# Optimization experiments

Hardware: AMD Instinct MI355X
Metric: run time of the kernel (lower is better)

The kernel has to match this reference:

```python
import jax, jax.numpy as jnp
import numpy as np

N_HEADS = 12


def setup_inputs() -> dict:
    key = jax.random.key(0)
    ks = jax.random.split(key, 3)
    B, N, C = 32, 1024, 768
    x = jax.random.normal(ks[0], (B, N, C), dtype=jnp.float32)
    w_qkv = jax.random.normal(ks[1], (C, 3 * C), dtype=jnp.float32) * (1.0 / np.sqrt(C))
    b_qkv = jnp.zeros((3 * C,), dtype=jnp.float32)
    w_out = jax.random.normal(ks[2], (C, C), dtype=jnp.float32) * (1.0 / np.sqrt(C))
    b_out = jnp.zeros((C,), dtype=jnp.float32)
    return {"x": x, "w_qkv": w_qkv, "b_qkv": b_qkv, "w_out": w_out, "b_out": b_out}


def reference(x, w_qkv, b_qkv, w_out, b_out):
    B, N, C = x.shape
    H = N_HEADS
    D = C // H  # head_dim
    qkv = (x @ w_qkv + b_qkv).reshape(B, N, 3, H, D)
    qkv = jnp.transpose(qkv, (2, 0, 3, 1, 4))
    q, k, v = qkv[0], qkv[1], qkv[2]
    # channel attention: k^T @ v -> (B,H,D,D), scaled by sqrt(head_dim)
    attn = jnp.einsum("bhnd,bhne->bhde", k, v) / np.sqrt(D).astype(np.float32)
    attn = jax.nn.softmax(attn, axis=-1)
    # attn @ q^T -> (B,H,D,N); swapaxes -> (B,H,N,D)
    out = jnp.einsum("bhde,bhne->bhnd", attn, q)
    # ProjOut: merge heads (B,N,C) + Dense(C)
    out = jnp.transpose(out, (0, 2, 1, 3)).reshape(B, N, C)
    return out @ w_out + b_out
```

## Files before the change

kernel.cpp:

```cpp
#include <hip/hip_runtime.h>
#include <hip/hip_bf16.h>
#include <stdint.h>
#include <stddef.h>

#define B_ 32
#define N_ 1024
#define C_ 768
#define H_ 12
#define D_ 64
#define M_ (B_*N_)
#define TC_ (3*C_)

typedef __bf16 bf16_t;
typedef __attribute__((ext_vector_type(8))) __bf16 bf16x8;
typedef __attribute__((ext_vector_type(4))) __bf16 bf16x4;
typedef __attribute__((ext_vector_type(4))) float  f32x4;

#define MFMA16(a,b,c) __builtin_amdgcn_mfma_f32_16x16x32_bf16(a,b,c,0,0,0)

__device__ __forceinline__ void lds_load16(const void* g, void* l) {
  __builtin_amdgcn_global_load_lds(
      (const __attribute__((address_space(1))) void*)g,
      (__attribute__((address_space(3))) void*)l, 16, 0, 0);
}

__global__ void cvt_bf16(const float* __restrict__ in, bf16_t* __restrict__ out, int n) {
  int i = (blockIdx.x * 256 + threadIdx.x) * 8;
  if (i >= n) return;
  const float4 a = *(const float4*)(in + i);
  const float4 b = *(const float4*)(in + i + 4);
  bf16x8 r;
  r[0]=(bf16_t)a.x; r[1]=(bf16_t)a.y; r[2]=(bf16_t)a.z; r[3]=(bf16_t)a.w;
  r[4]=(bf16_t)b.x; r[5]=(bf16_t)b.y; r[6]=(bf16_t)b.z; r[7]=(bf16_t)b.w;
  *(bf16x8*)(out + i) = r;
}

__global__ void transpose_cvt(const float* __restrict__ in, bf16_t* __restrict__ out,
                              int R, int Cc) {
  __shared__ float t[32][33];
  const int c0 = blockIdx.x * 32, r0 = blockIdx.y * 32;
  const int tx = threadIdx.x & 31, ty = threadIdx.x >> 5;
  #pragma unroll
  for (int k = 0; k < 4; ++k)
    t[ty + k*8][tx] = in[(size_t)(r0 + ty + k*8)*Cc + c0 + tx];
  __syncthreads();
  #pragma unroll
  for (int k = 0; k < 4; ++k)
    out[(size_t)(c0 + ty + k*8)*R + r0 + tx] = (bf16_t)t[tx][ty + k*8];
}

template<int MODE>
__global__ __launch_bounds__(512, 2)
void gemm_bt(const bf16_t* __restrict__ A, const bf16_t* __restrict__ BT,
             const float* __restrict__ bias, float* __restrict__ Cout,
             bf16_t* __restrict__ qh,
             bf16_t* __restrict__ kthi, bf16_t* __restrict__ vthi,
             int nbx)
{
  __shared__ __align__(16) char smem[131072];

  const int nwg = gridDim.x;
  const int cpx = nwg >> 3;
  const int bid = blockIdx.x;
  const int swz = (bid & 7) * cpx + (bid >> 3);
  const int bx  = swz % nbx;
  const int by  = swz / nbx;

  const int tid  = threadIdx.x;
  const int wave = tid >> 6;
  const int lane = tid & 63;
  const int rowBase = by * 256;
  const int colBase = bx * 256;
  const int wr = wave >> 2;
  const int wc = wave & 3;
  const int fr = lane & 15;
  const int b   = rowBase >> 10;
  const int nn0 = rowBase & (N_ - 1);

  const int srow = tid >> 2;
  const int scol = (((tid & 3) ^ ((tid >> 2) & 3)) << 3);
  const bf16_t *Ap0, *Ap1, *Bp0, *Bp1;
  if (MODE == 3) {
    Ap0 = A + (size_t)b * (H_*N_*D_) + (size_t)(nn0 + srow) * D_ + scol;
    Ap1 = Ap0 + (size_t)128 * D_;
    const size_t bts = (size_t)b * C_ * C_;
    Bp0 = BT + bts + (size_t)(colBase + srow) * 768 + scol;
    Bp1 = Bp0 + (size_t)128 * 768;
  } else {
    Ap0 = A + (size_t)(rowBase + srow) * 768 + scol;
    Ap1 = Ap0 + (size_t)128 * 768;
    Bp0 = BT + (size_t)(colBase + srow) * 768 + scol;
    Bp1 = Bp0 + (size_t)128 * 768;
  }

  const int chxA = (((lane >> 4) ^ (fr & 3)) << 4);
  const int aoff = (wr*128 + fr)*64 + chxA;
  const int boff = 16384 + (wc*64 + fr)*64 + chxA;

#define RDA(BI,MM) (*(const bf16x8*)(smem + (BI)*32768 + aoff + (MM)*1024))
#define RDB(BI,NN) (*(const bf16x8*)(smem + (BI)*32768 + boff + (NN)*1024))

#define A_OFF(K0) ((MODE == 3) ? ((size_t)((K0) >> 6) << 16) + ((K0) & 32) : (size_t)(K0))

#define STAGE_A(BI, T) do {                                                   \
    const int k0_ = (T) * 32;                                                 \
    const size_t ao_ = A_OFF(k0_);                                            \
    lds_load16(Ap0 + ao_, smem + (BI)*32768 + tid*16);                        \
    lds_load16(Ap1 + ao_, smem + (BI)*32768 + 8192 + tid*16);                 \
  } while (0)

#define STAGE_B(BI, T) do {                                                   \
    const int k0_ = (T) * 32;                                                 \
    lds_load16(Bp0 + k0_, smem + (BI)*32768 + 16384 + tid*16);                \
    lds_load16(Bp1 + k0_, smem + (BI)*32768 + 24576 + tid*16);                \
  } while (0)

  f32x4 acc[8][4];
  #pragma unroll
  for (int m = 0; m < 8; ++m)
    #pragma unroll
    for (int n = 0; n < 4; ++n) acc[m][n] = f32x4{0.f,0.f,0.f,0.f};

#define MFMA_HALF(MB)                                                         \
    acc[MB+0][0]=MFMA16(a0_,b0_,acc[MB+0][0]); acc[MB+0][1]=MFMA16(a0_,b1_,acc[MB+0][1]); \
    acc[MB+0][2]=MFMA16(a0_,b2_,acc[MB+0][2]); acc[MB+0][3]=MFMA16(a0_,b3_,acc[MB+0][3]); \
    acc[MB+1][0]=MFMA16(a1_,b0_,acc[MB+1][0]); acc[MB+1][1]=MFMA16(a1_,b1_,acc[MB+1][1]); \
    acc[MB+1][2]=MFMA16(a1_,b2_,acc[MB+1][2]); acc[MB+1][3]=MFMA16(a1_,b3_,acc[MB+1][3]); \
    acc[MB+2][0]=MFMA16(a2_,b0_,acc[MB+2][0]); acc[MB+2][1]=MFMA16(a2_,b1_,acc[MB+2][1]); \
    acc[MB+2][2]=MFMA16(a2_,b2_,acc[MB+2][2]); acc[MB+2][3]=MFMA16(a2_,b3_,acc[MB+2][3]); \
    acc[MB+3][0]=MFMA16(a3_,b0_,acc[MB+3][0]); acc[MB+3][1]=MFMA16(a3_,b1_,acc[MB+3][1]); \
    acc[MB+3][2]=MFMA16(a3_,b2_,acc[MB+3][2]); acc[MB+3][3]=MFMA16(a3_,b3_,acc[MB+3][3]);

#define TILE(BI, T, DOST, VM) do {                                            \
    asm volatile("s_waitcnt vmcnt(" #VM ")" ::: "memory");                    \
    __builtin_amdgcn_sched_barrier(0);                                        \
    __builtin_amdgcn_s_barrier();                                             \
    __builtin_amdgcn_sched_barrier(0);                                        \
    if (DOST) { STAGE_A(((BI)+3)&3, (T)+3); }                                 \
    __builtin_amdgcn_sched_barrier(0);                                        \
    bf16x8 b0_=RDB(BI,0), b1_=RDB(BI,1), b2_=RDB(BI,2), b3_=RDB(BI,3);        \
    bf16x8 a0_=RDA(BI,0), a1_=RDA(BI,1), a2_=RDA(BI,2), a3_=RDA(BI,3);        \
    __builtin_amdgcn_s_setprio(1);                                            \
    MFMA_HALF(0)                                                              \
    __builtin_amdgcn_s_setprio(0);                                            \
    if (DOST) { STAGE_B(((BI)+3)&3, (T)+3); }                                 \
    __builtin_amdgcn_sched_barrier(0);                                        \
    a0_=RDA(BI,4); a1_=RDA(BI,5); a2_=RDA(BI,6); a3_=RDA(BI,7);               \
    __builtin_amdgcn_s_setprio(1);                                            \
    MFMA_HALF(4)                                                              \
    __builtin_amdgcn_s_setprio(0);                                            \
    asm volatile("s_waitcnt lgkmcnt(0)" ::: "memory");                        \
    __builtin_amdgcn_sched_barrier(0);                                        \
  } while (0)

  STAGE_A(0,0); STAGE_B(0,0);
  STAGE_A(1,1); STAGE_B(1,1);
  STAGE_A(2,2); STAGE_B(2,2);

  #pragma unroll 1
  for (int t = 0; t < 20; t += 4) {
    TILE(0, t,   1, 8);
    TILE(1, t+1, 1, 8);
    TILE(2, t+2, 1, 8);
    TILE(3, t+3, 1, 8);
  }
  TILE(0, 20, 1, 8);
  TILE(1, 21, 0, 8);
  TILE(2, 22, 0, 4);
  TILE(3, 23, 0, 0);

#undef TILE
#undef MFMA_HALF
#undef STAGE_A
#undef STAGE_B
#undef A_OFF
#undef RDA
#undef RDB

  if (MODE == 3) {
    #pragma unroll
    for (int n = 0; n < 4; ++n) {
      const int gc = colBase + wc*64 + n*16 + fr;
      const float bb = bias[gc];
      #pragma unroll
      for (int m = 0; m < 8; ++m) {
        const int gr = rowBase + wr*128 + m*16 + ((lane >> 4) << 2);
        #pragma unroll
        for (int j = 0; j < 4; ++j)
          Cout[(size_t)(gr + j)*C_ + gc] = acc[m][n][j] + bb;
      }
    }
  } else {
    __syncthreads();
    bf16_t* tile = (bf16_t*)smem;
    const int s = colBase / C_;
    #pragma unroll 1
    for (int ch = 0; ch < 4; ++ch) {
      if (ch) __syncthreads();
      if (wc == ch) {
        #pragma unroll
        for (int n = 0; n < 4; ++n) {
          const int cl = n*16 + fr;
          const float bb = bias[colBase + ch*64 + cl];
          #pragma unroll
          for (int m = 0; m < 8; ++m) {
            const int r0 = wr*128 + m*16 + ((lane >> 4) << 2);
            bf16x4 hv;
            hv[0]=(bf16_t)(acc[m][n][0]+bb); hv[1]=(bf16_t)(acc[m][n][1]+bb);
            hv[2]=(bf16_t)(acc[m][n][2]+bb); hv[3]=(bf16_t)(acc[m][n][3]+bb);
            *(bf16x4*)&tile[cl*260 + r0] = hv;
          }
        }
      }
      __syncthreads();
      const int gcol0 = colBase + ch*64;
      if (s == 0) {
        const int h = gcol0 >> 6;
        const int r = tid >> 1, hh = tid & 1;
        bf16_t* dst = qh + (((size_t)b*H_ + h)*N_ + nn0 + r)*D_ + hh*32;
        #pragma unroll
        for (int i0 = 0; i0 < 32; i0 += 8) {
          bf16x8 vv;
          #pragma unroll
          for (int i = 0; i < 8; ++i) vv[i] = tile[(hh*32 + i0 + i)*260 + r];
          *(bf16x8*)&dst[i0] = vv;
        }
      } else {
        const int rem = gcol0 - s*C_;
        const int h = rem >> 6;
        const int d = tid >> 3, nq = (tid & 7)*32;
        bf16_t* dst = (s == 1 ? kthi : vthi)
                      + (((size_t)b*H_ + h)*D_ + d)*N_ + nn0 + nq;
        #pragma unroll
        for (int i0 = 0; i0 < 32; i0 += 8)
          *(bf16x8*)&dst[i0] = *(const bf16x8*)&tile[d*260 + nq + i0];
      }
    }
  }
}

__global__ __launch_bounds__(256, 2)
void attn_softmax_k(const bf16_t* __restrict__ kthi, const bf16_t* __restrict__ vthi,
                    bf16_t* __restrict__ attnT)
{
  __shared__ float tile[64][65];
  __shared__ float invs[64];
  const int bh = blockIdx.x;
  const int tid = threadIdx.x, wave = tid >> 6, lane = tid & 63;
  const int fr = lane & 15, fo = (lane >> 4) * 8;
  const size_t base = (size_t)bh * D_ * N_;
  f32x4 acc[4][4] = {{0.f,0.f,0.f,0.f}};
  const int k0lo = wave * 256;
  #pragma unroll 1
  for (int k0 = k0lo; k0 < k0lo + 256; k0 += 32) {
    bf16x8 ah[4], bhv[4];
    #pragma unroll
    for (int m = 0; m < 4; ++m)
      ah[m] = *(const bf16x8*)&kthi[base + (size_t)(m*16 + fr)*N_ + k0 + fo];
    #pragma unroll
    for (int n = 0; n < 4; ++n)
      bhv[n] = *(const bf16x8*)&vthi[base + (size_t)(n*16 + fr)*N_ + k0 + fo];
    #pragma unroll
    for (int m = 0; m < 4; ++m)
      #pragma unroll
      for (int n = 0; n < 4; ++n)
        acc[m][n] = MFMA16(ah[m], bhv[n], acc[m][n]);
  }
  for (int w = 0; w < 4; ++w) {
    if (wave == w) {
      #pragma unroll
      for (int m = 0; m < 4; ++m)
        #pragma unroll
        for (int n = 0; n < 4; ++n) {
          const int row = m*16 + ((lane >> 4) << 2);
          const int col = n*16 + fr;
          #pragma unroll
          for (int j = 0; j < 4; ++j) {
            if (w == 0) tile[row+j][col]  = acc[m][n][j];
            else        tile[row+j][col] += acc[m][n][j];
          }
        }
    }
    __syncthreads();
  }
  if (tid < 64) {
    float mx = -3.0e38f;
    #pragma unroll
    for (int c = 0; c < 64; ++c) mx = fmaxf(mx, tile[tid][c]);
    mx *= 0.125f;
    float ssum = 0.f;
    #pragma unroll
    for (int c = 0; c < 64; ++c) {
      const float ev = __expf(tile[tid][c]*0.125f - mx);
      tile[tid][c] = ev;
      ssum += ev;
    }
    invs[tid] = 1.0f / ssum;
  }
  __syncthreads();
  if (tid < 64) {
    bf16_t* ao = attnT + (size_t)bh * D_ * D_ + tid * D_;
    #pragma unroll
    for (int d0 = 0; d0 < 64; d0 += 8) {
      bf16x8 vv;
      #pragma unroll
      for (int i = 0; i < 8; ++i) vv[i] = (bf16_t)(tile[d0+i][tid] * invs[d0+i]);
      *(bf16x8*)&ao[d0] = vv;
    }
  }
}

__global__ __launch_bounds__(256, 2)
void compose_w2(const bf16_t* __restrict__ woutT, const bf16_t* __restrict__ attnT,
                bf16_t* __restrict__ w2t)
{
  const int jb = blockIdx.x;
  const int bh = blockIdx.y;
  const int b = bh / H_, h = bh - b*H_;
  const int tid = threadIdx.x, wave = tid >> 6, lane = tid & 63;
  const int fr = lane & 15, fo = (lane >> 4) * 8;
  const bf16_t* at = attnT + (size_t)bh * D_ * D_;
  f32x4 acc[2][4] = {{0.f,0.f,0.f,0.f}};
  #pragma unroll
  for (int kk = 0; kk < 2; ++kk) {
    bf16x8 af[2], bfv[4];
    #pragma unroll
    for (int m = 0; m < 2; ++m)
      af[m] = *(const bf16x8*)&woutT[(size_t)(jb*128 + wave*32 + m*16 + fr)*C_ + h*64 + kk*32 + fo];
    #pragma unroll
    for (int n = 0; n < 4; ++n)
      bfv[n] = *(const bf16x8*)&at[(n*16 + fr)*64 + kk*32 + fo];
    #pragma unroll
    for (int m = 0; m < 2; ++m)
      #pragma unroll
      for (int n = 0; n < 4; ++n)
        acc[m][n] = MFMA16(af[m], bfv[n], acc[m][n]);
  }
  bf16_t* wb = w2t + (size_t)b * C_ * C_;
  #pragma unroll
  for (int m = 0; m < 2; ++m) {
    const int j = jb*128 + wave*32 + m*16 + ((lane >> 4) << 2);
    #pragma unroll
    for (int n = 0; n < 4; ++n) {
      const int e = n*16 + fr;
      #pragma unroll
      for (int jj = 0; jj < 4; ++jj)
        wb[(size_t)(j + jj)*C_ + h*64 + e] = (bf16_t)acc[m][n][jj];
    }
  }
}

extern "C" void kernel_launch(void* const* d_in, const int* in_sizes, int n_in,
                              void* d_out, int out_size, void* d_ws, size_t ws_size,
                              hipStream_t stream)
{
  (void)in_sizes; (void)n_in; (void)out_size;
  const float* x     = (const float*)d_in[0];
  const float* w_qkv = (const float*)d_in[1];
  const float* b_qkv = (const float*)d_in[2];
  const float* w_out = (const float*)d_in[3];
  const float* b_out = (const float*)d_in[4];
  float* out = (float*)d_out;

  const size_t sz_xb   = (size_t)M_*C_*2;
  const size_t sz_wq   = (size_t)TC_*C_*2;
  const size_t sz_wo   = (size_t)C_*C_*2;
  const size_t sz_qh   = (size_t)B_*H_*N_*D_*2;
  const size_t sz_kv   = (size_t)B_*H_*D_*N_*2;
  const size_t sz_attn = (size_t)B_*H_*D_*D_*2;

  char* p = (char*)d_ws;
  bf16_t* xb    = (bf16_t*)p; p += sz_xb;
  bf16_t* wqkvT = (bf16_t*)p; p += sz_wq;
  bf16_t* woutT = (bf16_t*)p; p += sz_wo;
  bf16_t* qh    = (bf16_t*)p; p += sz_qh;
  bf16_t* kthi  = (bf16_t*)p; p += sz_kv;
  bf16_t* vthi  = (bf16_t*)p; p += sz_kv;
  bf16_t* attnT = (bf16_t*)p; p += sz_attn;
  const size_t base_need = (size_t)(p - (char*)d_ws);
  bf16_t* w2t = xb;

  if (ws_size < base_need) return;

  cvt_bf16<<<dim3((M_*C_)/2048), 256, 0, stream>>>(x, xb, M_*C_);
  transpose_cvt<<<dim3(TC_/32, C_/32), 256, 0, stream>>>(w_qkv, wqkvT, C_, TC_);
  transpose_cvt<<<dim3(C_/32,  C_/32), 256, 0, stream>>>(w_out, woutT, C_, C_);

  gemm_bt<1><<<dim3((TC_/256)*(M_/256)), 512, 0, stream>>>(
      xb, wqkvT, b_qkv, nullptr, qh, kthi, vthi, TC_/256);

  attn_softmax_k<<<dim3(B_*H_), 256, 0, stream>>>(kthi, vthi, attnT);

  compose_w2<<<dim3(C_/128, B_*H_), 256, 0, stream>>>(woutT, attnT, w2t);

  gemm_bt<3><<<dim3((C_/256)*(M_/256)), 512, 0, stream>>>(
      qh, w2t, b_out, out, nullptr, nullptr, nullptr, C_/256);
}
```

Baseline: 315.5 us.

## Load GEMM B operand directly to registers and shrink LDS to three A stages

The B operand (weights) is no longer staged through LDS. Each wave loads its B fragments straight from global memory into registers, double-buffered across tiles, while A keeps a three-stage LDS ring with a new swizzle. LDS use drops from 128KB to 48KB and the launch-bounds occupancy hint is removed, which is meant to cut LDS traffic and allow more resident workgroups. In exchange there are redundant global loads of B across the waves that share a column, higher VGPR pressure, and waits that are now placed differently inside the tile.

```diff
diff --git a/kernel.cpp b/kernel.cpp
--- a/kernel.cpp
+++ b/kernel.cpp
@@ -22,6 +22,12 @@
   __builtin_amdgcn_global_load_lds(
       (const __attribute__((address_space(1))) void*)g,
       (__attribute__((address_space(3))) void*)l, 16, 0, 0);
+}
+
+__device__ __forceinline__ bf16x8 gload16(const bf16_t* p) {
+  bf16x8 r;
+  asm volatile("global_load_dwordx4 %0, %1, off" : "=v"(r) : "v"(p));
+  return r;
 }
 
 __global__ void cvt_bf16(const float* __restrict__ in, bf16_t* __restrict__ out, int n) {
@@ -50,14 +56,14 @@
 }
 
 template<int MODE>
-__global__ __launch_bounds__(512, 2)
+__global__ __launch_bounds__(512)
 void gemm_bt(const bf16_t* __restrict__ A, const bf16_t* __restrict__ BT,
              const float* __restrict__ bias, float* __restrict__ Cout,
              bf16_t* __restrict__ qh,
              bf16_t* __restrict__ kthi, bf16_t* __restrict__ vthi,
              int nbx)
 {
-  __shared__ __align__(16) char smem[131072];
+  __shared__ __align__(16) char smem[49152];
 
   const int nwg = gridDim.x;
   const int cpx = nwg >> 3;
@@ -74,46 +80,54 @@
   const int wr = wave >> 2;
   const int wc = wave & 3;
   const int fr = lane & 15;
+  const int hi = lane >> 4;
   const int b   = rowBase >> 10;
   const int nn0 = rowBase & (N_ - 1);
 
   const int srow = tid >> 2;
-  const int scol = (((tid & 3) ^ ((tid >> 2) & 3)) << 3);
-  const bf16_t *Ap0, *Ap1, *Bp0, *Bp1;
+  const int scol = (((tid & 3) ^ ((tid >> 3) & 3)) << 3);
+  const bf16_t *Ap0, *Ap1;
   if (MODE == 3) {
     Ap0 = A + (size_t)b * (H_*N_*D_) + (size_t)(nn0 + srow) * D_ + scol;
     Ap1 = Ap0 + (size_t)128 * D_;
-    const size_t bts = (size_t)b * C_ * C_;
-    Bp0 = BT + bts + (size_t)(colBase + srow) * 768 + scol;
-    Bp1 = Bp0 + (size_t)128 * 768;
   } else {
     Ap0 = A + (size_t)(rowBase + srow) * 768 + scol;
     Ap1 = Ap0 + (size_t)128 * 768;
-    Bp0 = BT + (size_t)(colBase + srow) * 768 + scol;
-    Bp1 = Bp0 + (size_t)128 * 768;
-  }
-
-  const int chxA = (((lane >> 4) ^ (fr & 3)) << 4);
+  }
+
+  const bf16_t *Bq0, *Bq1, *Bq2, *Bq3;
+  {
+    const size_t bts = (MODE == 3) ? (size_t)b * C_ * C_ : 0;
+    const int bcol = colBase + wc*64 + fr;
+    const int ko = hi * 8;
+    Bq0 = BT + bts + (size_t)(bcol +  0)*768 + ko;
+    Bq1 = BT + bts + (size_t)(bcol + 16)*768 + ko;
+    Bq2 = BT + bts + (size_t)(bcol + 32)*768 + ko;
+    Bq3 = BT + bts + (size_t)(bcol + 48)*768 + ko;
+  }
+
+  const int chxA = ((hi ^ ((fr >> 1) & 3)) << 4);
   const int aoff = (wr*128 + fr)*64 + chxA;
-  const int boff = 16384 + (wc*64 + fr)*64 + chxA;
-
-#define RDA(BI,MM) (*(const bf16x8*)(smem + (BI)*32768 + aoff + (MM)*1024))
-#define RDB(BI,NN) (*(const bf16x8*)(smem + (BI)*32768 + boff + (NN)*1024))
+
+#define RDA(BI,MM) (*(const bf16x8*)(smem + (BI)*16384 + aoff + (MM)*1024))
 
 #define A_OFF(K0) ((MODE == 3) ? ((size_t)((K0) >> 6) << 16) + ((K0) & 32) : (size_t)(K0))
 
 #define STAGE_A(BI, T) do {                                                   \
     const int k0_ = (T) * 32;                                                 \
     const size_t ao_ = A_OFF(k0_);                                            \
-    lds_load16(Ap0 + ao_, smem + (BI)*32768 + tid*16);                        \
-    lds_load16(Ap1 + ao_, smem + (BI)*32768 + 8192 + tid*16);                 \
+    lds_load16(Ap0 + ao_, smem + (BI)*16384 + tid*16);                        \
+    lds_load16(Ap1 + ao_, smem + (BI)*16384 + 8192 + tid*16);                 \
   } while (0)
 
-#define STAGE_B(BI, T) do {                                                   \
-    const int k0_ = (T) * 32;                                                 \
-    lds_load16(Bp0 + k0_, smem + (BI)*32768 + 16384 + tid*16);                \
-    lds_load16(Bp1 + k0_, smem + (BI)*32768 + 24576 + tid*16);                \
+#define BLOAD(NS) do {                                                        \
+    NS##0 = gload16(Bq0); NS##1 = gload16(Bq1);                               \
+    NS##2 = gload16(Bq2); NS##3 = gload16(Bq3);                               \
+    Bq0 += 32; Bq1 += 32; Bq2 += 32; Bq3 += 32;                               \
   } while (0)
+
+  bf16x8 bsa0, bsa1, bsa2, bsa3;
+  bf16x8 bsb0, bsb1, bsb2, bsb3;
 
   f32x4 acc[8][4];
   #pragma unroll
@@ -121,61 +135,67 @@
     #pragma unroll
     for (int n = 0; n < 4; ++n) acc[m][n] = f32x4{0.f,0.f,0.f,0.f};
 
-#define MFMA_HALF(MB)                                                         \
-    acc[MB+0][0]=MFMA16(a0_,b0_,acc[MB+0][0]); acc[MB+0][1]=MFMA16(a0_,b1_,acc[MB+0][1]); \
-    acc[MB+0][2]=MFMA16(a0_,b2_,acc[MB+0][2]); acc[MB+0][3]=MFMA16(a0_,b3_,acc[MB+0][3]); \
-    acc[MB+1][0]=MFMA16(a1_,b0_,acc[MB+1][0]); acc[MB+1][1]=MFMA16(a1_,b1_,acc[MB+1][1]); \
-    acc[MB+1][2]=MFMA16(a1_,b2_,acc[MB+1][2]); acc[MB+1][3]=MFMA16(a1_,b3_,acc[MB+1][3]); \
-    acc[MB+2][0]=MFMA16(a2_,b0_,acc[MB+2][0]); acc[MB+2][1]=MFMA16(a2_,b1_,acc[MB+2][1]); \
-    acc[MB+2][2]=MFMA16(a2_,b2_,acc[MB+2][2]); acc[MB+2][3]=MFMA16(a2_,b3_,acc[MB+2][3]); \
-    acc[MB+3][0]=MFMA16(a3_,b0_,acc[MB+3][0]); acc[MB+3][1]=MFMA16(a3_,b1_,acc[MB+3][1]); \
-    acc[MB+3][2]=MFMA16(a3_,b2_,acc[MB+3][2]); acc[MB+3][3]=MFMA16(a3_,b3_,acc[MB+3][3]);
-
-#define TILE(BI, T, DOST, VM) do {                                            \
+#define MFMA_HALF(CS, MB)                                                     \
+    acc[MB+0][0]=MFMA16(a0_,CS##0,acc[MB+0][0]); acc[MB+0][1]=MFMA16(a0_,CS##1,acc[MB+0][1]); \
+    acc[MB+0][2]=MFMA16(a0_,CS##2,acc[MB+0][2]); acc[MB+0][3]=MFMA16(a0_,CS##3,acc[MB+0][3]); \
+    acc[MB+1][0]=MFMA16(a1_,CS##0,acc[MB+1][0]); acc[MB+1][1]=MFMA16(a1_,CS##1,acc[MB+1][1]); \
+    acc[MB+1][2]=MFMA16(a1_,CS##2,acc[MB+1][2]); acc[MB+1][3]=MFMA16(a1_,CS##3,acc[MB+1][3]); \
+    acc[MB+2][0]=MFMA16(a2_,CS##0,acc[MB+2][0]); acc[MB+2][1]=MFMA16(a2_,CS##1,acc[MB+2][1]); \
+    acc[MB+2][2]=MFMA16(a2_,CS##2,acc[MB+2][2]); acc[MB+2][3]=MFMA16(a2_,CS##3,acc[MB+2][3]); \
+    acc[MB+3][0]=MFMA16(a3_,CS##0,acc[MB+3][0]); acc[MB+3][1]=MFMA16(a3_,CS##1,acc[MB+3][1]); \
+    acc[MB+3][2]=MFMA16(a3_,CS##2,acc[MB+3][2]); acc[MB+3][3]=MFMA16(a3_,CS##3,acc[MB+3][3]);
+
+#define TILE(BI, NBI, CS, NS, T, DOB, DOA, VM) do {                           \
     asm volatile("s_waitcnt vmcnt(" #VM ")" ::: "memory");                    \
     __builtin_amdgcn_sched_barrier(0);                                        \
     __builtin_amdgcn_s_barrier();                                             \
     __builtin_amdgcn_sched_barrier(0);                                        \
-    if (DOST) { STAGE_A(((BI)+3)&3, (T)+3); }                                 \
-    __builtin_amdgcn_sched_barrier(0);                                        \
-    bf16x8 b0_=RDB(BI,0), b1_=RDB(BI,1), b2_=RDB(BI,2), b3_=RDB(BI,3);        \
+    if (DOB) { BLOAD(NS); }                                                   \
+    __builtin_amdgcn_sched_barrier(0);                                        \
+    if (DOA) { STAGE_A(NBI, (T)+2); }                                         \
+    __builtin_amdgcn_sched_barrier(0);                                        \
     bf16x8 a0_=RDA(BI,0), a1_=RDA(BI,1), a2_=RDA(BI,2), a3_=RDA(BI,3);        \
+    asm volatile("s_waitcnt lgkmcnt(0)" ::: "memory");                        \
+    __builtin_amdgcn_sched_barrier(0);                                        \
     __builtin_amdgcn_s_setprio(1);                                            \
-    MFMA_HALF(0)                                                              \
+    MFMA_HALF(CS, 0)                                                          \
     __builtin_amdgcn_s_setprio(0);                                            \
-    if (DOST) { STAGE_B(((BI)+3)&3, (T)+3); }                                 \
-    __builtin_amdgcn_sched_barrier(0);                                        \
     a0_=RDA(BI,4); a1_=RDA(BI,5); a2_=RDA(BI,6); a3_=RDA(BI,7);               \
+    asm volatile("s_waitcnt lgkmcnt(0)" ::: "memory");                        \
+    __builtin_amdgcn_sched_barrier(0);                                        \
     __builtin_amdgcn_s_setprio(1);                                            \
-    MFMA_HALF(4)                                                              \
+    MFMA_HALF(CS, 4)                                                          \
     __builtin_amdgcn_s_setprio(0);                                            \
-    asm volatile("s_waitcnt lgkmcnt(0)" ::: "memory");                        \
     __builtin_amdgcn_sched_barrier(0);                                        \
   } while (0)
 
-  STAGE_A(0,0); STAGE_B(0,0);
-  STAGE_A(1,1); STAGE_B(1,1);
-  STAGE_A(2,2); STAGE_B(2,2);
+  BLOAD(bsa);
+  STAGE_A(0, 0);
+  STAGE_A(1, 1);
 
   #pragma unroll 1
-  for (int t = 0; t < 20; t += 4) {
-    TILE(0, t,   1, 8);
-    TILE(1, t+1, 1, 8);
-    TILE(2, t+2, 1, 8);
-    TILE(3, t+3, 1, 8);
-  }
-  TILE(0, 20, 1, 8);
-  TILE(1, 21, 0, 8);
-  TILE(2, 22, 0, 4);
-  TILE(3, 23, 0, 0);
+  for (int it = 0; it < 3; ++it) {
+    const int tb = it * 6;
+    TILE(0, 2, bsa, bsb, tb+0, 1, 1, 2);
+    TILE(1, 0, bsb, bsa, tb+1, 1, 1, 2);
+    TILE(2, 1, bsa, bsb, tb+2, 1, 1, 2);
+    TILE(0, 2, bsb, bsa, tb+3, 1, 1, 2);
+    TILE(1, 0, bsa, bsb, tb+4, 1, 1, 2);
+    TILE(2, 1, bsb, bsa, tb+5, 1, 1, 2);
+  }
+  TILE(0, 2, bsa, bsb, 18, 1, 1, 2);
+  TILE(1, 0, bsb, bsa, 19, 1, 1, 2);
+  TILE(2, 1, bsa, bsb, 20, 1, 1, 2);
+  TILE(0, 2, bsb, bsa, 21, 1, 1, 2);
+  TILE(1, 0, bsa, bsb, 22, 1, 0, 2);
+  TILE(2, 1, bsb, bsa, 23, 0, 0, 0);
 
 #undef TILE
 #undef MFMA_HALF
+#undef BLOAD
 #undef STAGE_A
-#undef STAGE_B
 #undef A_OFF
 #undef RDA
-#undef RDB
 
   if (MODE == 3) {
     #pragma unroll
```

Result: slower. 366.1 us (+16.0%).
